# Kernel optimization log

Measured on AMD Instinct MI355X. Metric: run time of the kernel, lower is better.

## Reference

```python
import jax, jax.numpy as jnp
import numpy as np

N_NODES = 50000
N_EDGES = 800000
IN_DIM, HID_DIM, N_CLASS = 128, 128, 2
DROPOUT_P = 0.5
NEG_SLOPE = 0.01  # F.leaky_relu default


def gcn_conv(x, src, dst, W, b, n_nodes):
    """PyG GCNConv: add self-loops, sym-normalize, aggregate, then bias."""
    loops = jnp.arange(n_nodes, dtype=src.dtype)
    s = jnp.concatenate([src, loops])
    d = jnp.concatenate([dst, loops])
    # degree on A + I (edge weights = 1), counted at destination
    deg = jax.ops.segment_sum(jnp.ones_like(d, dtype=x.dtype), d, num_segments=n_nodes)
    dis = jnp.where(deg > 0, jax.lax.rsqrt(deg), 0.0)  # deg^{-1/2}
    norm = dis[s] * dis[d]                               # [E+N]
    h = x @ W                                            # [N, out]
    msg = h[s] * norm[:, None]                           # gather + scale
    out = jax.ops.segment_sum(msg, d, num_segments=n_nodes)  # scatter-add
    return out + b


def dropout(x, p, key):
    keep = 1.0 - p
    mask = jax.random.bernoulli(key, keep, x.shape)
    return jnp.where(mask, x / keep, 0.0)


def setup_inputs() -> dict:
    key = jax.random.key(0)
    ks = jax.random.split(key, 8)
    x = jax.random.normal(ks[0], (N_NODES, IN_DIM), dtype=jnp.float32)
    edge_index = jax.random.randint(ks[1], (2, N_EDGES), 0, N_NODES, dtype=jnp.int64)
    def glorot(k, fin, fout):
        lim = np.sqrt(6.0 / (fin + fout)).astype(np.float32)
        return jax.random.uniform(k, (fin, fout), jnp.float32, -lim, lim)
    W1 = glorot(ks[2], IN_DIM, HID_DIM)
    W2 = glorot(ks[3], HID_DIM, HID_DIM)
    W3 = glorot(ks[4], HID_DIM, N_CLASS)
    b1 = jnp.zeros((HID_DIM,), jnp.float32)
    b2 = jnp.zeros((HID_DIM,), jnp.float32)
    b3 = jnp.zeros((N_CLASS,), jnp.float32)
    return {"x": x, "edge_index": edge_index, "W1": W1, "b1": b1,
            "W2": W2, "b2": b2, "W3": W3, "b3": b3}


def reference(x, edge_index, W1, b1, W2, b2, W3, b3):
    src, dst = edge_index[0], edge_index[1]
    n = x.shape[0]
    dkey = jax.random.key(42)
    k1, k2 = jax.random.split(dkey)
    h = gcn_conv(x, src, dst, W1, b1, n)
    h = jax.nn.leaky_relu(h, NEG_SLOPE)
    h = dropout(h, DROPOUT_P, k1)
    h = gcn_conv(h, src, dst, W2, b2, n)
    h = jax.nn.leaky_relu(h, NEG_SLOPE)
    h = dropout(h, DROPOUT_P, k2)
    h = gcn_conv(h, src, dst, W3, b3, n)
    return jax.nn.log_softmax(h, axis=1)
```

## Files before the change

### kernel.cpp

```cpp
#include <hip/hip_runtime.h>
#include <stdint.h>

#define N_NODES 50000
#define N_EDGES 800000
#define DIM     128
#define NB   196
#define CAP  8192
#define CHUNK 2048
#define NBLK 391
#define GNODES 16
#define GGRID 3125
#define GCAP 2048
#define G3NODES 128
#define G3CAP 4096
#define ZBLK 98

typedef __attribute__((ext_vector_type(8))) unsigned short ushort8_t;
typedef __attribute__((ext_vector_type(8))) short bfrag;
typedef __attribute__((ext_vector_type(4))) float f32x4;

__host__ __device__ inline void threefry2x32(uint32_t k0, uint32_t k1,
                                             uint32_t x0, uint32_t x1,
                                             uint32_t& o0, uint32_t& o1) {
    uint32_t ks0 = k0, ks1 = k1, ks2 = k0 ^ k1 ^ 0x1BD11BDAu;
    uint32_t v0 = x0 + ks0, v1 = x1 + ks1;
#define TF_R(r) { v0 += v1; v1 = (v1 << (r)) | (v1 >> (32 - (r))); v1 ^= v0; }
    TF_R(13) TF_R(15) TF_R(26) TF_R(6)
    v0 += ks1; v1 += ks2 + 1u;
    TF_R(17) TF_R(29) TF_R(16) TF_R(24)
    v0 += ks2; v1 += ks0 + 2u;
    TF_R(13) TF_R(15) TF_R(26) TF_R(6)
    v0 += ks0; v1 += ks1 + 3u;
    TF_R(17) TF_R(29) TF_R(16) TF_R(24)
    v0 += ks1; v1 += ks2 + 4u;
    TF_R(13) TF_R(15) TF_R(26) TF_R(6)
    v0 += ks2; v1 += ks0 + 5u;
#undef TF_R
    o0 = v0; o1 = v1;
}

__device__ inline float drop_scale(uint32_t kk0, uint32_t kk1, uint32_t i) {
    uint32_t b0, b1;
    threefry2x32(kk0, kk1, 0u, i, b0, b1);
    uint32_t bits = b0 ^ b1;
    return (bits >> 31) ? 0.0f : 2.0f;
}

__device__ inline float bf2f(ushort u) {
    return __uint_as_float(((uint32_t)u) << 16);
}
__device__ inline float bfpair_lo(uint32_t u) { return __uint_as_float(u << 16); }
__device__ inline float bfpair_hi(uint32_t u) { return __uint_as_float(u & 0xffff0000u); }

__device__ inline ushort f2bf_rne(float f) {
    uint32_t bits = __float_as_uint(f);
    uint32_t lsb = (bits >> 16) & 1u;
    bits += 0x7fffu + lsb;
    return (ushort)(bits >> 16);
}

__device__ inline void acc8(float* acc, uint4 u, float d) {
    acc[0] += d * bfpair_lo(u.x); acc[1] += d * bfpair_hi(u.x);
    acc[2] += d * bfpair_lo(u.y); acc[3] += d * bfpair_hi(u.y);
    acc[4] += d * bfpair_lo(u.z); acc[5] += d * bfpair_hi(u.z);
    acc[6] += d * bfpair_lo(u.w); acc[7] += d * bfpair_hi(u.w);
}
__device__ inline void acc8p(float* acc, uint4 u) {
    acc[0] += bfpair_lo(u.x); acc[1] += bfpair_hi(u.x);
    acc[2] += bfpair_lo(u.y); acc[3] += bfpair_hi(u.y);
    acc[4] += bfpair_lo(u.z); acc[5] += bfpair_hi(u.z);
    acc[6] += bfpair_lo(u.w); acc[7] += bfpair_hi(u.w);
}

template<int F32A, int SCALE>
__device__ inline void gemm_body(const ushort* __restrict__ Xb,
                                 const float* __restrict__ Xf,
                                 const ushort* __restrict__ Wt,
                                 const float* __restrict__ dis,
                                 ushort* __restrict__ Hb, int gb, int tid) {
    int w = tid >> 6, lane = tid & 63;
    int m0 = gb * 128 + w * 32;
    int lrow = lane & 15, quad = lane >> 4;
    f32x4 acc[2][8] = {};
    for (int kt = 0; kt < DIM; kt += 32) {
        bfrag a[2], b[8];
        #pragma unroll
        for (int t = 0; t < 2; ++t) {
            int m = m0 + t * 16 + lrow;
            if (m >= N_NODES) m = 0;
            if (F32A) {
                const float* p = Xf + (size_t)m * DIM + kt + quad * 8;
                f32x4 v0 = *(const f32x4*)p;
                f32x4 v1 = *(const f32x4*)(p + 4);
                #pragma unroll
                for (int j = 0; j < 4; ++j) {
                    a[t][j]     = (short)f2bf_rne(v0[j]);
                    a[t][j + 4] = (short)f2bf_rne(v1[j]);
                }
            } else {
                a[t] = *(const bfrag*)(Xb + (size_t)m * DIM + kt + quad * 8);
            }
        }
        #pragma unroll
        for (int c = 0; c < 8; ++c) {
            int n = c * 16 + lrow;
            b[c] = *(const bfrag*)(Wt + (size_t)n * DIM + kt + quad * 8);
        }
        #pragma unroll
        for (int t = 0; t < 2; ++t)
            #pragma unroll
            for (int c = 0; c < 8; ++c)
                acc[t][c] = __builtin_amdgcn_mfma_f32_16x16x32_bf16(a[t], b[c], acc[t][c], 0, 0, 0);
    }
    #pragma unroll
    for (int t = 0; t < 2; ++t) {
        #pragma unroll
        for (int r = 0; r < 4; ++r) {
            int rowi = m0 + t * 16 + quad * 4 + r;
            if (rowi < N_NODES) {
                float dv = SCALE ? dis[rowi] : 1.0f;
                #pragma unroll
                for (int c = 0; c < 8; ++c) {
                    int feat = c * 16 + lrow;
                    float z = SCALE ? acc[t][c][r] * dv : acc[t][c][r];
                    Hb[(size_t)rowi * DIM + feat] = f2bf_rne(z);
                }
            }
        }
    }
}

__global__ __launch_bounds__(256) void k_prep(const float* __restrict__ W1,
                                              const float* __restrict__ W2,
                                              ushort* __restrict__ W1t,
                                              ushort* __restrict__ W2t,
                                              const int* __restrict__ src,
                                              const int* __restrict__ dst,
                                              uint32_t* __restrict__ gcur,
                                              uint32_t* __restrict__ packed,
                                              float* __restrict__ h3s) {
    __shared__ uint32_t h[NB];
    int b = blockIdx.x;
    int t = threadIdx.x;
    if (b < NBLK) {
        uint32_t dc[CHUNK / 256], sc[CHUNK / 256];
        if (t < NB) h[t] = 0u;
        __syncthreads();
        int base = b * CHUNK;
        #pragma unroll
        for (int i = 0; i < CHUNK / 256; ++i) {
            int e = base + i * 256 + t;
            if (e < N_EDGES) {
                dc[i] = (uint32_t)dst[e];
                sc[i] = (uint32_t)src[e];
                atomicAdd(&h[dc[i] >> 8], 1u);
            } else {
                dc[i] = 0xffffffffu;
            }
        }
        __syncthreads();
        if (t < NB) {
            uint32_t c = h[t];
            h[t] = c ? atomicAdd(&gcur[t], c) : 0u;
        }
        __syncthreads();
        #pragma unroll
        for (int i = 0; i < CHUNK / 256; ++i) {
            if (dc[i] != 0xffffffffu) {
                uint32_t d = dc[i];
                uint32_t s = sc[i];
                uint32_t bk = d >> 8;
                uint32_t pos = atomicAdd(&h[bk], 1u);
                if (pos < CAP)
                    packed[(size_t)bk * CAP + pos] = ((d & 255u) << 16) | s;
            }
        }
    } else if (b < NBLK + 128) {
        int j = (b - NBLK) * 256 + t;
        const float* W = (j < DIM * DIM) ? W1 : W2;
        ushort* Wt = (j < DIM * DIM) ? W1t : W2t;
        int i = j & (DIM * DIM - 1);
        int k = i >> 7, n = i & 127;
        Wt[n * DIM + k] = f2bf_rne(W[k * DIM + n]);
    } else {
        int idx = (b - NBLK - 128) * 256 + t;
        if (idx < (N_NODES * 2) / 4) {
            f32x4 z = {0.f, 0.f, 0.f, 0.f};
            ((f32x4*)h3s)[idx] = z;
        }
    }
}

__global__ __launch_bounds__(256) void k_fill(const uint32_t* __restrict__ gcur,
                                              const uint32_t* __restrict__ packed,
                                              uint32_t* __restrict__ row,
                                              float* __restrict__ dis,
                                              ushort* __restrict__ col16,
                                              const float* __restrict__ x,
                                              const ushort* __restrict__ W1t,
                                              ushort* __restrict__ Hb) {
    __shared__ uint32_t sdeg[256];
    __shared__ uint32_t scan[256];
    __shared__ uint32_t cur[256];
    int b = blockIdx.x;
    int t = threadIdx.x;
    if (b >= NB) {
        gemm_body<1, 0>(nullptr, x, W1t, nullptr, Hb, b - NB, t);
        return;
    }
    uint32_t n = gcur[b];
    scan[t] = (t < b) ? gcur[t] : 0u;
    __syncthreads();
    for (int off = 1; off < 256; off <<= 1) {
        uint32_t xx = (t >= off) ? scan[t - off] : 0u;
        __syncthreads();
        scan[t] += xx;
        __syncthreads();
    }
    uint32_t cbase = scan[255];
    __syncthreads();
    uint32_t pbase = (uint32_t)b * CAP;
    sdeg[t] = 0u;
    __syncthreads();
    for (uint32_t i = t; i < n; i += 256) {
        uint32_t u = packed[pbase + i];
        atomicAdd(&sdeg[u >> 16], 1u);
    }
    __syncthreads();
    uint32_t myd = sdeg[t];
    scan[t] = myd;
    __syncthreads();
    for (int off = 1; off < 256; off <<= 1) {
        uint32_t xx = (t >= off) ? scan[t - off] : 0u;
        __syncthreads();
        scan[t] += xx;
        __syncthreads();
    }
    uint32_t excl = scan[t] - myd;
    cur[t] = excl;
    int v = b * 256 + t;
    if (v <= N_NODES) row[v] = cbase + excl;
    if (v < N_NODES)  dis[v] = 1.0f / sqrtf((float)(myd + 1u));
    __syncthreads();
    for (uint32_t i = t; i < n; i += 256) {
        uint32_t u = packed[pbase + i];
        uint32_t pos = cbase + atomicAdd(&cur[u >> 16], 1u);
        col16[pos] = (ushort)(u & 0xffffu);
    }
}

__global__ __launch_bounds__(256) void k_fused(const uint32_t* __restrict__ row,
                                               const ushort* __restrict__ col16,
                                               const float* __restrict__ dis,
                                               const ushort* __restrict__ Hb,
                                               const float* __restrict__ bias,
                                               const ushort* __restrict__ W2t,
                                               ushort* __restrict__ Hb2,
                                               uint32_t kk0, uint32_t kk1) {
    __shared__ ushort scol[GCAP];
    __shared__ uint32_t srow[GNODES + 1];
    __shared__ ushort At[GNODES * DIM];
    int tid = threadIdx.x;
    int nbase = blockIdx.x * GNODES;
    if (tid <= GNODES) srow[tid] = row[nbase + tid];
    __syncthreads();
    uint32_t eLo = srow[0];
    uint32_t count = srow[GNODES] - eLo;
    bool staged = count <= GCAP;
    if (staged) {
        for (uint32_t i = tid; i < count; i += 256) scol[i] = col16[eLo + i];
    }
    __syncthreads();

    int nl = tid >> 4;
    int q  = tid & 15;
    int v = nbase + nl;
    float dv = dis[v];
    float acc[8];
    {
        uint4 u = *(const uint4*)(Hb + (size_t)v * DIM + q * 8);
        acc[0] = bfpair_lo(u.x); acc[1] = bfpair_hi(u.x);
        acc[2] = bfpair_lo(u.y); acc[3] = bfpair_hi(u.y);
        acc[4] = bfpair_lo(u.z); acc[5] = bfpair_hi(u.z);
        acc[6] = bfpair_lo(u.w); acc[7] = bfpair_hi(u.w);
        #pragma unroll
        for (int j = 0; j < 8; ++j) acc[j] *= dv;
    }
    uint32_t e0 = srow[nl] - eLo, e1 = srow[nl + 1] - eLo;
    uint32_t e = e0;
    if (staged) {
        for (; e + 8 <= e1; e += 8) {
            uint32_t s0 = scol[e],     s1 = scol[e + 1];
            uint32_t s2 = scol[e + 2], s3 = scol[e + 3];
            uint32_t s4 = scol[e + 4], s5 = scol[e + 5];
            uint32_t s6 = scol[e + 6], s7 = scol[e + 7];
            uint4 u0 = *(const uint4*)(Hb + (size_t)s0 * DIM + q * 8);
            uint4 u1 = *(const uint4*)(Hb + (size_t)s1 * DIM + q * 8);
            uint4 u2 = *(const uint4*)(Hb + (size_t)s2 * DIM + q * 8);
            uint4 u3 = *(const uint4*)(Hb + (size_t)s3 * DIM + q * 8);
            uint4 u4 = *(const uint4*)(Hb + (size_t)s4 * DIM + q * 8);
            uint4 u5 = *(const uint4*)(Hb + (size_t)s5 * DIM + q * 8);
            uint4 u6 = *(const uint4*)(Hb + (size_t)s6 * DIM + q * 8);
            uint4 u7 = *(const uint4*)(Hb + (size_t)s7 * DIM + q * 8);
            float d0 = dis[s0], d1 = dis[s1], d2 = dis[s2], d3 = dis[s3];
            float d4 = dis[s4], d5 = dis[s5], d6 = dis[s6], d7 = dis[s7];
            acc8(acc, u0, d0); acc8(acc, u1, d1);
            acc8(acc, u2, d2); acc8(acc, u3, d3);
            acc8(acc, u4, d4); acc8(acc, u5, d5);
            acc8(acc, u6, d6); acc8(acc, u7, d7);
        }
        for (; e + 4 <= e1; e += 4) {
            uint32_t s0 = scol[e],     s1 = scol[e + 1];
            uint32_t s2 = scol[e + 2], s3 = scol[e + 3];
            uint4 u0 = *(const uint4*)(Hb + (size_t)s0 * DIM + q * 8);
            uint4 u1 = *(const uint4*)(Hb + (size_t)s1 * DIM + q * 8);
            uint4 u2 = *(const uint4*)(Hb + (size_t)s2 * DIM + q * 8);
            uint4 u3 = *(const uint4*)(Hb + (size_t)s3 * DIM + q * 8);
            float d0 = dis[s0], d1 = dis[s1], d2 = dis[s2], d3 = dis[s3];
            acc8(acc, u0, d0); acc8(acc, u1, d1);
            acc8(acc, u2, d2); acc8(acc, u3, d3);
        }
        for (; e < e1; ++e) {
            uint32_t s0 = scol[e];
            uint4 u0 = *(const uint4*)(Hb + (size_t)s0 * DIM + q * 8);
            acc8(acc, u0, dis[s0]);
        }
    } else {
        for (; e < e1; ++e) {
            uint32_t s0 = col16[eLo + e];
            uint4 u0 = *(const uint4*)(Hb + (size_t)s0 * DIM + q * 8);
            acc8(acc, u0, dis[s0]);
        }
    }
    {
        int cbase = q * 8;
        uint32_t ibase = (uint32_t)(v * DIM + cbase);
        ushort8_t o;
        #pragma unroll
        for (int j = 0; j < 8; ++j) {
            float z = acc[j] * dv + bias[cbase + j];
            z = (z >= 0.f) ? z : 0.01f * z;
            z *= drop_scale(kk0, kk1, ibase + j);
            o[j] = f2bf_rne(z);
        }
        *((ushort8_t*)(At + nl * DIM + ((q * 8) ^ ((nl & 7) << 3)))) = o;
    }
    __syncthreads();

    int w = tid >> 6, lane = tid & 63;
    int lrow = lane & 15, quad = lane >> 4;
    int swz = (lrow & 7) << 3;
    f32x4 acc2[2] = {};
    for (int kt = 0; kt < DIM; kt += 32) {
        int k = kt + quad * 8;
        bfrag a = *(const bfrag*)(At + lrow * DIM + (k ^ swz));
        #pragma unroll
        for (int ct = 0; ct < 2; ++ct) {
            int n = (w * 2 + ct) * 16 + lrow;
            bfrag b = *(const bfrag*)(W2t + (size_t)n * DIM + k);
            acc2[ct] = __builtin_amdgcn_mfma_f32_16x16x32_bf16(a, b, acc2[ct], 0, 0, 0);
        }
    }
    #pragma unroll
    for (int ct = 0; ct < 2; ++ct) {
        #pragma unroll
        for (int rr = 0; rr < 4; ++rr) {
            int rowi = nbase + quad * 4 + rr;
            float dvv = dis[rowi];
            int feat = (w * 2 + ct) * 16 + lrow;
            Hb2[(size_t)rowi * DIM + feat] = f2bf_rne(acc2[ct][rr] * dvv);
        }
    }
}

__global__ __launch_bounds__(256) void k_gather2(const uint32_t* __restrict__ row,
                                                 const ushort* __restrict__ col16,
                                                 const float* __restrict__ dis,
                                                 const ushort* __restrict__ Hb,
                                                 const float* __restrict__ bias,
                                                 const float* __restrict__ W3,
                                                 float* __restrict__ h3s,
                                                 uint32_t kk0, uint32_t kk1) {
    __shared__ ushort scol[GCAP];
    __shared__ uint32_t srow[GNODES + 1];
    int tid = threadIdx.x;
    int nbase = blockIdx.x * GNODES;
    if (tid <= GNODES) srow[tid] = row[nbase + tid];
    __syncthreads();
    uint32_t eLo = srow[0];
    uint32_t count = srow[GNODES] - eLo;
    bool staged = count <= GCAP;
    if (staged) {
        for (uint32_t i = tid; i < count; i += 256) scol[i] = col16[eLo + i];
    }
    __syncthreads();

    int nl = tid >> 4;
    int q  = tid & 15;
    int v = nbase + nl;
    float dv = dis[v];
    float acc[8];
    {
        uint4 u = *(const uint4*)(Hb + (size_t)v * DIM + q * 8);
        acc[0] = bfpair_lo(u.x); acc[1] = bfpair_hi(u.x);
        acc[2] = bfpair_lo(u.y); acc[3] = bfpair_hi(u.y);
        acc[4] = bfpair_lo(u.z); acc[5] = bfpair_hi(u.z);
        acc[6] = bfpair_lo(u.w); acc[7] = bfpair_hi(u.w);
    }

    uint32_t e0 = srow[nl] - eLo, e1 = srow[nl + 1] - eLo;
    uint32_t e = e0;
    if (staged) {
        for (; e + 8 <= e1; e += 8) {
            uint32_t s0 = scol[e],     s1 = scol[e + 1];
            uint32_t s2 = scol[e + 2], s3 = scol[e + 3];
            uint32_t s4 = scol[e + 4], s5 = scol[e + 5];
            uint32_t s6 = scol[e + 6], s7 = scol[e + 7];
            uint4 u0 = *(const uint4*)(Hb + (size_t)s0 * DIM + q * 8);
            uint4 u1 = *(const uint4*)(Hb + (size_t)s1 * DIM + q * 8);
            uint4 u2 = *(const uint4*)(Hb + (size_t)s2 * DIM + q * 8);
            uint4 u3 = *(const uint4*)(Hb + (size_t)s3 * DIM + q * 8);
            uint4 u4 = *(const uint4*)(Hb + (size_t)s4 * DIM + q * 8);
            uint4 u5 = *(const uint4*)(Hb + (size_t)s5 * DIM + q * 8);
            uint4 u6 = *(const uint4*)(Hb + (size_t)s6 * DIM + q * 8);
            uint4 u7 = *(const uint4*)(Hb + (size_t)s7 * DIM + q * 8);
            acc8p(acc, u0); acc8p(acc, u1); acc8p(acc, u2); acc8p(acc, u3);
            acc8p(acc, u4); acc8p(acc, u5); acc8p(acc, u6); acc8p(acc, u7);
        }
        for (; e + 4 <= e1; e += 4) {
            uint32_t s0 = scol[e],     s1 = scol[e + 1];
            uint32_t s2 = scol[e + 2], s3 = scol[e + 3];
            uint4 u0 = *(const uint4*)(Hb + (size_t)s0 * DIM + q * 8);
            uint4 u1 = *(const uint4*)(Hb + (size_t)s1 * DIM + q * 8);
            uint4 u2 = *(const uint4*)(Hb + (size_t)s2 * DIM + q * 8);
            uint4 u3 = *(const uint4*)(Hb + (size_t)s3 * DIM + q * 8);
            acc8p(acc, u0); acc8p(acc, u1); acc8p(acc, u2); acc8p(acc, u3);
        }
        for (; e < e1; ++e) {
            uint4 u0 = *(const uint4*)(Hb + (size_t)scol[e] * DIM + q * 8);
            acc8p(acc, u0);
        }
    } else {
        for (; e < e1; ++e) {
            uint4 u0 = *(const uint4*)(Hb + (size_t)col16[eLo + e] * DIM + q * 8);
            acc8p(acc, u0);
        }
    }

    int cbase = q * 8;
    uint32_t ibase = (uint32_t)(v * DIM + cbase);
    float o0 = 0.f, o1 = 0.f;
    #pragma unroll
    for (int j = 0; j < 8; ++j) {
        float z = acc[j] * dv + bias[cbase + j];
        z = (z >= 0.f) ? z : 0.01f * z;
        z *= drop_scale(kk0, kk1, ibase + j);
        o0 += z * W3[(cbase + j) * 2 + 0];
        o1 += z * W3[(cbase + j) * 2 + 1];
    }
    o0 += __shfl_xor(o0, 1); o0 += __shfl_xor(o0, 2);
    o0 += __shfl_xor(o0, 4); o0 += __shfl_xor(o0, 8);
    o1 += __shfl_xor(o1, 1); o1 += __shfl_xor(o1, 2);
    o1 += __shfl_xor(o1, 4); o1 += __shfl_xor(o1, 8);
    if (q == 0) {
        atomicAdd(&h3s[v * 2 + 0], o0 * dv);
        atomicAdd(&h3s[v * 2 + 1], o1 * dv);
    }
}

__global__ __launch_bounds__(256) void k_gather3(const uint32_t* __restrict__ row,
                                                 const ushort* __restrict__ col16,
                                                 const float* __restrict__ dis,
                                                 const float* __restrict__ H3s,
                                                 const float* __restrict__ b3,
                                                 float* __restrict__ out) {
    __shared__ ushort scol[G3CAP];
    __shared__ uint32_t srow[G3NODES + 1];
    int tid = threadIdx.x;
    int nbase = blockIdx.x * G3NODES;
    int nend = nbase + G3NODES; if (nend > N_NODES) nend = N_NODES;
    int nloc = nend - nbase;
    for (int i = tid; i <= nloc; i += 256) srow[i] = row[nbase + i];
    __syncthreads();
    uint32_t eLo = srow[0];
    uint32_t count = srow[nloc] - eLo;
    bool staged = count <= G3CAP;
    if (staged) {
        for (uint32_t i = tid; i < count; i += 256) scol[i] = col16[eLo + i];
    }
    __syncthreads();

    int nl = tid >> 1;
    int par = tid & 1;
    int v = nbase + nl;
    if (v >= N_NODES) return;
    const float2* H2 = (const float2*)H3s;
    float z0 = 0.f, z1 = 0.f;
    if (par == 0) {
        float2 h = H2[v];
        z0 = h.x; z1 = h.y;
    }
    uint32_t e0 = srow[nl] - eLo, e1 = srow[nl + 1] - eLo;
    if (staged) {
        for (uint32_t e = e0 + par; e < e1; e += 2) {
            float2 ha = H2[scol[e]];
            z0 += ha.x; z1 += ha.y;
        }
    } else {
        for (uint32_t e = e0 + par; e < e1; e += 2) {
            float2 ha = H2[col16[eLo + e]];
            z0 += ha.x; z1 += ha.y;
        }
    }
    z0 += __shfl_xor(z0, 1);
    z1 += __shfl_xor(z1, 1);
    if (par) return;
    float dv = dis[v];
    z0 = z0 * dv + b3[0];
    z1 = z1 * dv + b3[1];
    float m = fmaxf(z0, z1);
    float lse = m + logf(expf(z0 - m) + expf(z1 - m));
    out[v * 2 + 0] = z0 - lse;
    out[v * 2 + 1] = z1 - lse;
}

extern "C" void kernel_launch(void* const* d_in, const int* in_sizes, int n_in,
                              void* d_out, int out_size, void* d_ws, size_t ws_size,
                              hipStream_t stream) {
    const float* x  = (const float*)d_in[0];
    const int*   ei = (const int*)d_in[1];
    const float* W1 = (const float*)d_in[2];
    const float* b1 = (const float*)d_in[3];
    const float* W2 = (const float*)d_in[4];
    const float* b2 = (const float*)d_in[5];
    const float* W3 = (const float*)d_in[6];
    const float* b3 = (const float*)d_in[7];
    float* out = (float*)d_out;

    const int* src = ei;
    const int* dst = ei + N_EDGES;

    uint32_t* wsu = (uint32_t*)d_ws;
    float*    wsf = (float*)d_ws;
    uint32_t* gcur   = wsu;
    uint32_t* row    = wsu + 256;
    float*    dis    = wsf + 50304;
    uint32_t* packed = wsu + 100352;
    ushort*   col16  = (ushort*)(wsu + 1705984);
    ushort*   Hb     = (ushort*)(wsu + 2106112);
    ushort*   Hb2    = (ushort*)(wsu + 8506112);
    ushort*   W1t    = (ushort*)(wsu + 11706112);
    ushort*   W2t    = (ushort*)(wsu + 11714304);
    float*    h3s    = wsf + 11722496;

    uint32_t k1a, k1b, k2a, k2b;
    threefry2x32(0u, 42u, 0u, 0u, k1a, k1b);
    threefry2x32(0u, 42u, 0u, 1u, k2a, k2b);

    hipMemsetAsync(gcur, 0, 256 * sizeof(uint32_t), stream);

    k_prep<<<NBLK + 128 + ZBLK, 256, 0, stream>>>(W1, W2, W1t, W2t,
                                                  src, dst, gcur, packed, h3s);

    k_fill<<<NB + 391, 256, 0, stream>>>(gcur, packed, row, dis, col16,
                                         x, W1t, Hb);

    k_fused<<<GGRID, 256, 0, stream>>>(row, col16, dis, Hb, b1, W2t, Hb2,
                                       k1a, k1b);

    k_gather2<<<GGRID, 256, 0, stream>>>(row, col16, dis, Hb2, b2, W3, h3s,
                                         k2a, k2b);

    k_gather3<<<(N_NODES + G3NODES - 1) / G3NODES, 256, 0, stream>>>(row, col16, dis,
                                                                     h3s, b3, out);
}
```

Measured before the change: 204.2 us.

## Replace bucketed two-pass CSR build with global-atomic degree, scan, and fill

Drops the per-bucket packed staging buffer and its in-block histogram passes. CSR construction becomes three steps: global atomic degree counting, a per-block scan where each block re-sums all preceding degrees to get its base offset, and a fill pass that scatters src ids through global atomics on per-node cursors. The h3s zeroing moves into a single larger memset that also clears deg and cur. The cost is an extra kernel launch, heavy contention from random global atomics, an O(N) redundant prefix sum in each scan block, and column order within a row that is no longer deterministic.

```diff
diff --git a/kernel.cpp b/kernel.cpp
--- a/kernel.cpp
+++ b/kernel.cpp
@@ -4,16 +4,14 @@
 #define N_NODES 50000
 #define N_EDGES 800000
 #define DIM     128
-#define NB   196
-#define CAP  8192
-#define CHUNK 2048
-#define NBLK 391
+#define EBLK 782
+#define GEMM1BLK 391
 #define GNODES 16
 #define GGRID 3125
 #define GCAP 2048
 #define G3NODES 128
 #define G3CAP 4096
-#define ZBLK 98
+#define SCANBLK 196
 
 typedef __attribute__((ext_vector_type(8))) unsigned short ushort8_t;
 typedef __attribute__((ext_vector_type(8))) short bfrag;
@@ -130,86 +128,52 @@
     }
 }
 
-__global__ __launch_bounds__(256) void k_prep(const float* __restrict__ W1,
-                                              const float* __restrict__ W2,
-                                              ushort* __restrict__ W1t,
-                                              ushort* __restrict__ W2t,
-                                              const int* __restrict__ src,
-                                              const int* __restrict__ dst,
-                                              uint32_t* __restrict__ gcur,
-                                              uint32_t* __restrict__ packed,
-                                              float* __restrict__ h3s) {
-    __shared__ uint32_t h[NB];
+__global__ __launch_bounds__(256) void k_deg(const int* __restrict__ dst,
+                                             uint32_t* __restrict__ deg,
+                                             const float* __restrict__ W1,
+                                             const float* __restrict__ W2,
+                                             ushort* __restrict__ W1t,
+                                             ushort* __restrict__ W2t) {
     int b = blockIdx.x;
     int t = threadIdx.x;
-    if (b < NBLK) {
-        uint32_t dc[CHUNK / 256], sc[CHUNK / 256];
-        if (t < NB) h[t] = 0u;
-        __syncthreads();
-        int base = b * CHUNK;
-        #pragma unroll
-        for (int i = 0; i < CHUNK / 256; ++i) {
+    if (b < EBLK) {
+        int base = b * 1024;
+        #pragma unroll
+        for (int i = 0; i < 4; ++i) {
             int e = base + i * 256 + t;
-            if (e < N_EDGES) {
-                dc[i] = (uint32_t)dst[e];
-                sc[i] = (uint32_t)src[e];
-                atomicAdd(&h[dc[i] >> 8], 1u);
-            } else {
-                dc[i] = 0xffffffffu;
-            }
-        }
-        __syncthreads();
-        if (t < NB) {
-            uint32_t c = h[t];
-            h[t] = c ? atomicAdd(&gcur[t], c) : 0u;
-        }
-        __syncthreads();
-        #pragma unroll
-        for (int i = 0; i < CHUNK / 256; ++i) {
-            if (dc[i] != 0xffffffffu) {
-                uint32_t d = dc[i];
-                uint32_t s = sc[i];
-                uint32_t bk = d >> 8;
-                uint32_t pos = atomicAdd(&h[bk], 1u);
-                if (pos < CAP)
-                    packed[(size_t)bk * CAP + pos] = ((d & 255u) << 16) | s;
-            }
-        }
-    } else if (b < NBLK + 128) {
-        int j = (b - NBLK) * 256 + t;
+            if (e < N_EDGES) atomicAdd(&deg[(uint32_t)dst[e]], 1u);
+        }
+    } else {
+        int j = (b - EBLK) * 256 + t;
         const float* W = (j < DIM * DIM) ? W1 : W2;
         ushort* Wt = (j < DIM * DIM) ? W1t : W2t;
         int i = j & (DIM * DIM - 1);
         int k = i >> 7, n = i & 127;
         Wt[n * DIM + k] = f2bf_rne(W[k * DIM + n]);
-    } else {
-        int idx = (b - NBLK - 128) * 256 + t;
-        if (idx < (N_NODES * 2) / 4) {
-            f32x4 z = {0.f, 0.f, 0.f, 0.f};
-            ((f32x4*)h3s)[idx] = z;
-        }
-    }
-}
-
-__global__ __launch_bounds__(256) void k_fill(const uint32_t* __restrict__ gcur,
-                                              const uint32_t* __restrict__ packed,
+    }
+}
+
+__global__ __launch_bounds__(256) void k_scan(const uint32_t* __restrict__ deg,
                                               uint32_t* __restrict__ row,
-                                              float* __restrict__ dis,
-                                              ushort* __restrict__ col16,
-                                              const float* __restrict__ x,
-                                              const ushort* __restrict__ W1t,
-                                              ushort* __restrict__ Hb) {
-    __shared__ uint32_t sdeg[256];
+                                              uint32_t* __restrict__ cur,
+                                              float* __restrict__ dis) {
+    __shared__ uint32_t red[256];
     __shared__ uint32_t scan[256];
-    __shared__ uint32_t cur[256];
     int b = blockIdx.x;
     int t = threadIdx.x;
-    if (b >= NB) {
-        gemm_body<1, 0>(nullptr, x, W1t, nullptr, Hb, b - NB, t);
-        return;
-    }
-    uint32_t n = gcur[b];
-    scan[t] = (t < b) ? gcur[t] : 0u;
+    int nbase = b * 256;
+    uint32_t p = 0;
+    for (int i = t; i < nbase; i += 256) p += deg[i];
+    red[t] = p;
+    __syncthreads();
+    for (int off = 128; off > 0; off >>= 1) {
+        if (t < off) red[t] += red[t + off];
+        __syncthreads();
+    }
+    uint32_t cbase = red[0];
+    int v = nbase + t;
+    uint32_t myd = (v < N_NODES) ? deg[v] : 0u;
+    scan[t] = myd;
     __syncthreads();
     for (int off = 1; off < 256; off <<= 1) {
         uint32_t xx = (t >= off) ? scan[t - off] : 0u;
@@ -217,35 +181,37 @@
         scan[t] += xx;
         __syncthreads();
     }
-    uint32_t cbase = scan[255];
-    __syncthreads();
-    uint32_t pbase = (uint32_t)b * CAP;
-    sdeg[t] = 0u;
-    __syncthreads();
-    for (uint32_t i = t; i < n; i += 256) {
-        uint32_t u = packed[pbase + i];
-        atomicAdd(&sdeg[u >> 16], 1u);
-    }
-    __syncthreads();
-    uint32_t myd = sdeg[t];
-    scan[t] = myd;
-    __syncthreads();
-    for (int off = 1; off < 256; off <<= 1) {
-        uint32_t xx = (t >= off) ? scan[t - off] : 0u;
-        __syncthreads();
-        scan[t] += xx;
-        __syncthreads();
-    }
     uint32_t excl = scan[t] - myd;
-    cur[t] = excl;
-    int v = b * 256 + t;
     if (v <= N_NODES) row[v] = cbase + excl;
-    if (v < N_NODES)  dis[v] = 1.0f / sqrtf((float)(myd + 1u));
-    __syncthreads();
-    for (uint32_t i = t; i < n; i += 256) {
-        uint32_t u = packed[pbase + i];
-        uint32_t pos = cbase + atomicAdd(&cur[u >> 16], 1u);
-        col16[pos] = (ushort)(u & 0xffffu);
+    if (v < N_NODES) {
+        cur[v] = cbase + excl;
+        dis[v] = 1.0f / sqrtf((float)(myd + 1u));
+    }
+}
+
+__global__ __launch_bounds__(256) void k_fillcol(const int* __restrict__ src,
+                                                 const int* __restrict__ dst,
+                                                 uint32_t* __restrict__ cur,
+                                                 ushort* __restrict__ col16,
+                                                 const float* __restrict__ x,
+                                                 const ushort* __restrict__ W1t,
+                                                 ushort* __restrict__ Hb) {
+    int b = blockIdx.x;
+    int t = threadIdx.x;
+    if (b < EBLK) {
+        int base = b * 1024;
+        #pragma unroll
+        for (int i = 0; i < 4; ++i) {
+            int e = base + i * 256 + t;
+            if (e < N_EDGES) {
+                uint32_t d = (uint32_t)dst[e];
+                uint32_t s = (uint32_t)src[e];
+                uint32_t pos = atomicAdd(&cur[d], 1u);
+                col16[pos] = (ushort)s;
+            }
+        }
+    } else {
+        gemm_body<1, 0>(nullptr, x, W1t, nullptr, Hb, b - EBLK, t);
     }
 }
 
@@ -542,28 +508,29 @@
 
     uint32_t* wsu = (uint32_t*)d_ws;
     float*    wsf = (float*)d_ws;
-    uint32_t* gcur   = wsu;
-    uint32_t* row    = wsu + 256;
-    float*    dis    = wsf + 50304;
-    uint32_t* packed = wsu + 100352;
-    ushort*   col16  = (ushort*)(wsu + 1705984);
-    ushort*   Hb     = (ushort*)(wsu + 2106112);
-    ushort*   Hb2    = (ushort*)(wsu + 8506112);
-    ushort*   W1t    = (ushort*)(wsu + 11706112);
-    ushort*   W2t    = (ushort*)(wsu + 11714304);
-    float*    h3s    = wsf + 11722496;
+    uint32_t* deg    = wsu;
+    uint32_t* cur    = wsu + 50176;
+    float*    h3s    = wsf + 100352;
+    uint32_t* row    = wsu + 200448;
+    float*    dis    = wsf + 250752;
+    ushort*   col16  = (ushort*)(wsu + 300800);
+    ushort*   Hb     = (ushort*)(wsu + 700800);
+    ushort*   Hb2    = (ushort*)(wsu + 3900800);
+    ushort*   W1t    = (ushort*)(wsu + 7100800);
+    ushort*   W2t    = (ushort*)(wsu + 7108992);
 
     uint32_t k1a, k1b, k2a, k2b;
     threefry2x32(0u, 42u, 0u, 0u, k1a, k1b);
     threefry2x32(0u, 42u, 0u, 1u, k2a, k2b);
 
-    hipMemsetAsync(gcur, 0, 256 * sizeof(uint32_t), stream);
-
-    k_prep<<<NBLK + 128 + ZBLK, 256, 0, stream>>>(W1, W2, W1t, W2t,
-                                                  src, dst, gcur, packed, h3s);
-
-    k_fill<<<NB + 391, 256, 0, stream>>>(gcur, packed, row, dis, col16,
-                                         x, W1t, Hb);
+    hipMemsetAsync(wsu, 0, 200448 * sizeof(uint32_t), stream);
+
+    k_deg<<<EBLK + 128, 256, 0, stream>>>(dst, deg, W1, W2, W1t, W2t);
+
+    k_scan<<<SCANBLK, 256, 0, stream>>>(deg, row, cur, dis);
+
+    k_fillcol<<<EBLK + GEMM1BLK, 256, 0, stream>>>(src, dst, cur, col16,
+                                                   x, W1t, Hb);
 
     k_fused<<<GGRID, 256, 0, stream>>>(row, col16, dis, Hb, b1, W2t, Hb2,
                                        k1a, k1b);
```

Result: slower. 285.6 us (+39.9%).
